# Kernel optimization log

Hardware: AMD Instinct MI355X
Metric: run time of the kernel (lower is better)

## Reference

```python
import jax, jax.numpy as jnp
import numpy as np

B, N, L, C, H = 2, 3000, 6, 128, 1
IN_DIM = 6
SIGMA_D = 1.0
EPS = 1e-5
DH = C // H


def _conv1(x, W, b):
    # pointwise Conv1d: x [B,Cin,N], W [Cout,Cin], b [Cout]
    return jnp.einsum('oc,bcn->bon', W, x) + b[None, :, None]


def _bn(x, g, beta):
    # BatchNorm1d (training-mode batch stats) over (B, N) per channel
    m = x.mean(axis=(0, 2), keepdims=True)
    v = x.var(axis=(0, 2), keepdims=True)
    return g[None, :, None] * (x - m) * jax.lax.rsqrt(v + EPS) + beta[None, :, None]


def setup_inputs() -> dict:
    key = jax.random.key(0)
    ks = iter(jax.random.split(key, 80))

    def w(shape, fan_in):
        return jax.random.normal(next(ks), shape, jnp.float32) * (1.0 / np.sqrt(fan_in))

    src = jax.random.normal(next(ks), (B, N, 3), jnp.float32)
    tgt = src + 0.1 * jax.random.normal(next(ks), (B, N, 3), jnp.float32)
    corr_pos = jnp.concatenate([src, tgt], axis=-1)  # [B,N,6]

    d = {
        'corr_pos': corr_pos, 'src_keypts': src, 'tgt_keypts': tgt,
        'init_W': w((C, IN_DIM), IN_DIM), 'init_b': jnp.zeros((C,), jnp.float32),
        'pcn_W': w((L, C, C), C), 'pcn_b': jnp.zeros((L, C), jnp.float32),
        'pcn_g': jnp.ones((L, C), jnp.float32), 'pcn_beta': jnp.zeros((L, C), jnp.float32),
        'qW': w((L, C, C), C), 'qb': jnp.zeros((L, C), jnp.float32),
        'kW': w((L, C, C), C), 'kb': jnp.zeros((L, C), jnp.float32),
        'vW': w((L, C, C), C), 'vb': jnp.zeros((L, C), jnp.float32),
        'm1W': w((L, C // 2, C), C), 'm1b': jnp.zeros((L, C // 2), jnp.float32),
        'm1g': jnp.ones((L, C // 2), jnp.float32), 'm1beta': jnp.zeros((L, C // 2), jnp.float32),
        'm2W': w((L, C // 2, C // 2), C // 2), 'm2b': jnp.zeros((L, C // 2), jnp.float32),
        'm2g': jnp.ones((L, C // 2), jnp.float32), 'm2beta': jnp.zeros((L, C // 2), jnp.float32),
        'm3W': w((L, C, C // 2), C // 2), 'm3b': jnp.zeros((L, C), jnp.float32),
        'c1W': w((32, C), C), 'c1b': jnp.zeros((32,), jnp.float32),
        'c2W': w((32, 32), 32), 'c2b': jnp.zeros((32,), jnp.float32),
        'c3W': w((1, 32), 32), 'c3b': jnp.zeros((1,), jnp.float32),
    }
    return d


def reference(corr_pos, src_keypts, tgt_keypts, init_W, init_b,
              pcn_W, pcn_b, pcn_g, pcn_beta,
              qW, qb, kW, kb, vW, vb,
              m1W, m1b, m1g, m1beta, m2W, m2b, m2g, m2beta, m3W, m3b,
              c1W, c1b, c2W, c2b, c3W, c3b):
    # spatial compatibility: clamp(1 - (d_src - d_tgt)^2 / sigma_d^2, min=0)  [B,N,N]
    src_dist = jnp.linalg.norm(src_keypts[:, :, None, :] - src_keypts[:, None, :, :], axis=-1)
    tgt_dist = jnp.linalg.norm(tgt_keypts[:, :, None, :] - tgt_keypts[:, None, :, :], axis=-1)
    sc = jnp.maximum(1.0 - (src_dist - tgt_dist) ** 2 / SIGMA_D ** 2, 0.0)

    # init embedding: [B,C,N]
    x = _conv1(jnp.swapaxes(corr_pos, 1, 2), init_W, init_b)
    scale = 1.0 / jnp.sqrt(jnp.float32(DH))

    for i in range(L):
        # PointCN layer
        x = jax.nn.relu(_bn(_conv1(x, pcn_W[i], pcn_b[i]), pcn_g[i], pcn_beta[i]))
        # NonLocal block
        Q = _conv1(x, qW[i], qb[i]).reshape(B, H, DH, N)
        K = _conv1(x, kW[i], kb[i]).reshape(B, H, DH, N)
        V = _conv1(x, vW[i], vb[i]).reshape(B, H, DH, N)
        scores = jnp.einsum('bhco,bhci->bhoi', Q, K) * scale  # [B,H,N,N]
        weight = jax.nn.softmax(sc[:, None, :, :] * scores, axis=-1)
        msg = jnp.einsum('bhoi,bhci->bhco', weight, V).reshape(B, C, N)
        msg = jax.nn.relu(_bn(_conv1(msg, m1W[i], m1b[i]), m1g[i], m1beta[i]))
        msg = jax.nn.relu(_bn(_conv1(msg, m2W[i], m2b[i]), m2g[i], m2beta[i]))
        msg = _conv1(msg, m3W[i], m3b[i])
        x = x + msg

    corr_feat = x
    norm = jnp.maximum(jnp.linalg.norm(corr_feat, axis=1, keepdims=True), 1e-12)
    normed_corr_feat = corr_feat / norm
    h = jax.nn.relu(_conv1(corr_feat, c1W, c1b))
    h = jax.nn.relu(_conv1(h, c2W, c2b))
    confidence = _conv1(h, c3W, c3b)[:, 0, :]  # [B,N]
    return confidence, normed_corr_feat
```

## Files before the change

### kernel.cpp

```cpp
#include <hip/hip_runtime.h>
#include <hip/hip_bf16.h>


#define BB 2
#define NN 3000
#define CC 128
#define LAYERS 6
#define BN_EPS 1e-5f
#define ATT_SCALE 0.08838834764831845f
#define INV_CNT (1.f / (float)(BB * NN))

typedef _Float16 f16;
typedef _Float16 f16x8 __attribute__((ext_vector_type(8)));
typedef float f32x4 __attribute__((ext_vector_type(4)));

__global__ void init_conv(const float* __restrict__ corr, const float* __restrict__ W,
                          const float* __restrict__ bias, float* __restrict__ x) {
  int idx = blockIdx.x * 256 + threadIdx.x;
  if (idx >= BB * CC * NN) return;
  int n = idx % NN;
  int c = (idx / NN) % CC;
  int b = idx / (NN * CC);
  const float* cp = corr + (b * NN + n) * 6;
  float acc = bias[c];
#pragma unroll
  for (int d = 0; d < 6; ++d) acc += W[c * 6 + d] * cp[d];
  x[idx] = acc;
}

template <int CIN, int COUT, int MODE, int INPT, int CSPLIT, int BNIN, int STATS>
__launch_bounds__(256)
__global__ void conv_k(const float* __restrict__ in, float* __restrict__ out,
                       const float* __restrict__ W, const float* __restrict__ bias,
                       const float* __restrict__ res,
                       const float* __restrict__ isums, const float* __restrict__ ig,
                       const float* __restrict__ ibeta,
                       const float* __restrict__ rsums, const float* __restrict__ rg,
                       const float* __restrict__ rbeta, float* __restrict__ osums) {
  constexpr int COB = COUT / CSPLIT;
  constexpr int CH = (CIN > 64) ? 64 : CIN;
  constexpr int KPT = COB / 32;
  __shared__ alignas(16) float Xs[CIN][INPT ? 36 : 32];
  __shared__ float Ws[COB][CH + 1];
  __shared__ float bnsc[BNIN ? CIN : 1], bnsh[BNIN ? CIN : 1];
  const int tid = threadIdx.x;
  const int p0 = blockIdx.x * 32;
  const int co0 = blockIdx.y * COB;

  if (BNIN) {
    for (int c = tid; c < CIN; c += 256) {
      float s = isums[c], s2 = isums[CIN + c];
      float mean = s * INV_CNT;
      float var = s2 * INV_CNT - mean * mean;
      float sc = ig[c] * rsqrtf(var + BN_EPS);
      bnsc[c] = sc;
      bnsh[c] = ibeta[c] - mean * sc;
    }
    __syncthreads();
  }

  if (INPT == 0) {
    for (int idx = tid; idx < CIN * 32; idx += 256) {
      int ci = idx >> 5, j = idx & 31;
      int p = p0 + j;
      float v = 0.f;
      if (p < BB * NN) {
        int b = p / NN, n = p % NN;
        v = in[(b * CIN + ci) * NN + n];
        if (BNIN) {
          v = v * bnsc[ci] + bnsh[ci];
          v = v > 0.f ? v : 0.f;
        }
      }
      Xs[ci][j] = v;
    }
  } else {
    for (int idx = tid; idx < CIN * 32; idx += 256) {
      int j = idx / CIN, ci = idx % CIN;
      int p = p0 + j;
      float v = 0.f;
      if (p < BB * NN) {
        v = in[p * CIN + ci];
        if (BNIN) {
          v = v * bnsc[ci] + bnsh[ci];
          v = v > 0.f ? v : 0.f;
        }
      }
      Xs[ci][j] = v;
    }
  }

  const int nb = (tid % 8) * 4;
  const int cb = (tid / 8) * KPT;

  float acc[KPT][4];
#pragma unroll
  for (int k = 0; k < KPT; ++k)
#pragma unroll
    for (int j = 0; j < 4; ++j) acc[k][j] = 0.f;

  for (int c0 = 0; c0 < CIN; c0 += CH) {
    __syncthreads();
    for (int idx = tid; idx < COB * CH; idx += 256) {
      int co = idx / CH, cc = idx % CH;
      Ws[co][cc] = W[(co0 + co) * CIN + c0 + cc];
    }
    __syncthreads();
#pragma unroll 4
    for (int cc = 0; cc < CH; ++cc) {
      float4 xv = *reinterpret_cast<const float4*>(&Xs[c0 + cc][nb]);
#pragma unroll
      for (int k = 0; k < KPT; ++k) {
        float w = Ws[cb + k][cc];
        acc[k][0] += w * xv.x;
        acc[k][1] += w * xv.y;
        acc[k][2] += w * xv.z;
        acc[k][3] += w * xv.w;
      }
    }
  }

#pragma unroll
  for (int k = 0; k < KPT; ++k) {
    int co = co0 + cb + k;
    float bv = bias[co];
    float rsc = 0.f, rsh = 0.f;
    if (MODE == 3) {
      float s = rsums[co], s2 = rsums[COUT + co];
      float mean = s * INV_CNT;
      float var = s2 * INV_CNT - mean * mean;
      rsc = rg[co] * rsqrtf(var + BN_EPS);
      rsh = rbeta[co] - mean * rsc;
    }
    float sp = 0.f, sp2 = 0.f;
#pragma unroll
    for (int j = 0; j < 4; ++j) {
      int p = p0 + nb + j;
      if (p < BB * NN) {
        int b = p / NN, n = p % NN;
        int o = (b * COUT + co) * NN + n;
        float v = acc[k][j] + bv;
        if (MODE == 1) v = v > 0.f ? v : 0.f;
        if (MODE == 3) {
          float rr = res[o] * rsc + rsh;
          v += (rr > 0.f ? rr : 0.f);
        }
        out[o] = v;
        if (STATS) {
          sp += v;
          sp2 += v * v;
        }
      }
    }
    if (STATS) {
      sp += __shfl_xor(sp, 1);
      sp2 += __shfl_xor(sp2, 1);
      sp += __shfl_xor(sp, 2);
      sp2 += __shfl_xor(sp2, 2);
      sp += __shfl_xor(sp, 4);
      sp2 += __shfl_xor(sp2, 4);
      if ((tid & 7) == 0) {
        atomicAdd(&osums[co], sp);
        atomicAdd(&osums[COUT + co], sp2);
      }
    }
  }
}

__launch_bounds__(256)
__global__ void conv_qkv(const float* __restrict__ Yp, const float* __restrict__ psums,
                         const float* __restrict__ pg, const float* __restrict__ pbeta,
                         const float* __restrict__ qW, const float* __restrict__ kW,
                         const float* __restrict__ vW, const float* __restrict__ qb,
                         const float* __restrict__ kb, const float* __restrict__ vb,
                         f16* __restrict__ Qh, f16* __restrict__ Ql,
                         f16* __restrict__ Kh, f16* __restrict__ Kl,
                         f16* __restrict__ Vh, f16* __restrict__ Vl) {
  __shared__ alignas(16) float Xs[128][32];
  __shared__ float Ws[64][65];
  __shared__ float bnsc[128], bnsh[128];
  const int tid = threadIdx.x;
  const int p0 = blockIdx.x * 32;
  const int sel = blockIdx.y >> 1;
  const int co0 = (blockIdx.y & 1) * 64;
  const float* W = (sel == 0) ? qW : (sel == 1) ? kW : vW;
  const float* bias = (sel == 0) ? qb : (sel == 1) ? kb : vb;

  for (int c = tid; c < 128; c += 256) {
    float s = psums[c], s2 = psums[128 + c];
    float mean = s * INV_CNT;
    float var = s2 * INV_CNT - mean * mean;
    float sc = pg[c] * rsqrtf(var + BN_EPS);
    bnsc[c] = sc;
    bnsh[c] = pbeta[c] - mean * sc;
  }
  __syncthreads();

  for (int idx = tid; idx < 128 * 32; idx += 256) {
    int ci = idx >> 5, j = idx & 31;
    int p = p0 + j;
    float v = 0.f;
    if (p < BB * NN) {
      int b = p / NN, n = p % NN;
      v = Yp[(b * 128 + ci) * NN + n];
      v = v * bnsc[ci] + bnsh[ci];
      v = v > 0.f ? v : 0.f;
    }
    Xs[ci][j] = v;
  }

  const int nb = (tid % 8) * 4;
  const int cb = (tid / 8) * 2;
  float acc[2][4] = {{0.f, 0.f, 0.f, 0.f}, {0.f, 0.f, 0.f, 0.f}};

  for (int c0 = 0; c0 < 128; c0 += 64) {
    __syncthreads();
    for (int idx = tid; idx < 64 * 64; idx += 256) {
      int co = idx >> 6, cc = idx & 63;
      Ws[co][cc] = W[(co0 + co) * 128 + c0 + cc];
    }
    __syncthreads();
#pragma unroll 4
    for (int cc = 0; cc < 64; ++cc) {
      float4 xv = *reinterpret_cast<const float4*>(&Xs[c0 + cc][nb]);
#pragma unroll
      for (int k = 0; k < 2; ++k) {
        float w = Ws[cb + k][cc];
        acc[k][0] += w * xv.x;
        acc[k][1] += w * xv.y;
        acc[k][2] += w * xv.z;
        acc[k][3] += w * xv.w;
      }
    }
  }

#pragma unroll
  for (int k = 0; k < 2; ++k) {
    int co = co0 + cb + k;
    float bv = bias[co];
#pragma unroll
    for (int j = 0; j < 4; ++j) {
      int p = p0 + nb + j;
      if (p < BB * NN) {
        int b = p / NN, n = p % NN;
        float v = acc[k][j] + bv;
        f16 h = (f16)v;
        f16 lo = (f16)(v - (float)h);
        if (sel == 0) {
          size_t o = (size_t)(b * NN + n) * CC + co;
          Qh[o] = h; Ql[o] = lo;
        } else if (sel == 1) {
          size_t o = (size_t)(b * NN + n) * CC + co;
          Kh[o] = h; Kl[o] = lo;
        } else {
          size_t o = (size_t)(b * CC + co) * NN + n;
          Vh[o] = h; Vl[o] = lo;
        }
      }
    }
  }
}

__launch_bounds__(256)
__global__ void attn_mf6(const f16* __restrict__ Qhp, const f16* __restrict__ Qlp,
                         const f16* __restrict__ Khp, const f16* __restrict__ Klp,
                         const f16* __restrict__ Vhp, const f16* __restrict__ Vlp,
                         const float* __restrict__ srcp, const float* __restrict__ tgtp,
                         float* __restrict__ pacc, float* __restrict__ pm,
                         float* __restrict__ pl, int chunk) {
  const int b = blockIdx.z;
  const int q0 = blockIdx.x * 64;
  const int s = blockIdx.y;
  const int cs = s * chunk;
  const int ce = min(cs + chunk, NN);
  const int tid = threadIdx.x;
  const int w = tid >> 6, lane = tid & 63, quad = lane >> 4, l15 = lane & 15;

  __shared__ f16 Ksh[32][136], Ksl[32][136];
  __shared__ f16 Vsh[128][40], Vsl[128][40];
  __shared__ f16 Ps[4][16][40];
  __shared__ float kps[6][36];

  float qp[4][6];
  const int orow = q0 + w * 16;
#pragma unroll
  for (int r = 0; r < 4; ++r) {
    int o = orow + quad * 4 + r;
    if (o >= NN) o = NN - 1;
#pragma unroll
    for (int d = 0; d < 3; ++d) {
      qp[r][d] = srcp[(b * NN + o) * 3 + d];
      qp[r][3 + d] = tgtp[(b * NN + o) * 3 + d];
    }
  }
  f16x8 qh[4], ql[4];
  {
    int o = orow + l15;
    if (o >= NN) o = NN - 1;
    size_t base = (size_t)(b * NN + o) * CC + quad * 8;
#pragma unroll
    for (int cc = 0; cc < 4; ++cc) {
      qh[cc] = *reinterpret_cast<const f16x8*>(Qhp + base + cc * 32);
      ql[cc] = *reinterpret_cast<const f16x8*>(Qlp + base + cc * 32);
    }
  }

  float m[4], l[4];
#pragma unroll
  for (int r = 0; r < 4; ++r) {
    m[r] = -1e30f;
    l[r] = 0.f;
  }
  f32x4 acco[8];
#pragma unroll
  for (int t = 0; t < 8; ++t) acco[t] = (f32x4){0.f, 0.f, 0.f, 0.f};

  const int NT = (ce - cs + 31) >> 5;
  for (int it = 0; it < NT; ++it) {
    const int kk0 = cs + it * 32;
    __syncthreads();
    for (int t = tid; t < 1024; t += 256) {
      int plane = t >> 9, row = (t >> 4) & 31, cu = t & 15;
      int kr = kk0 + row;
      if (kr >= NN) kr = NN - 1;
      const f16* src = (plane ? Klp : Khp) + (size_t)(b * NN + kr) * CC + cu * 8;
      uint4 v = *reinterpret_cast<const uint4*>(src);
      f16* dst = plane ? &Ksl[row][cu * 8] : &Ksh[row][cu * 8];
      *reinterpret_cast<uint4*>(dst) = v;
    }
    for (int t = tid; t < 1024; t += 256) {
      int plane = t >> 9, c = (t >> 2) & 127, iu = t & 3;
      int kb = kk0 + iu * 8;
      if (kb > NN - 8) kb = NN - 8;
      const f16* src = (plane ? Vlp : Vhp) + (size_t)(b * CC + c) * NN + kb;
      uint4 v = *reinterpret_cast<const uint4*>(src);
      f16* dst = plane ? &Vsl[c][iu * 8] : &Vsh[c][iu * 8];
      *reinterpret_cast<uint4*>(dst) = v;
    }
    for (int t = tid; t < 192; t += 256) {
      int d = t >> 5, i = t & 31;
      int ig = kk0 + i;
      if (ig >= NN) ig = NN - 1;
      kps[d][i] = (d < 3) ? srcp[(b * NN + ig) * 3 + d] : tgtp[(b * NN + ig) * 3 + d - 3];
    }
    __syncthreads();

    f32x4 accs[2];
#pragma unroll
    for (int k4 = 0; k4 < 2; ++k4) accs[k4] = (f32x4){0.f, 0.f, 0.f, 0.f};
#pragma unroll
    for (int cc = 0; cc < 4; ++cc) {
#pragma unroll
      for (int k4 = 0; k4 < 2; ++k4) {
        f16x8 bh = *reinterpret_cast<const f16x8*>(&Ksh[k4 * 16 + l15][cc * 32 + quad * 8]);
        f16x8 bl = *reinterpret_cast<const f16x8*>(&Ksl[k4 * 16 + l15][cc * 32 + quad * 8]);
        accs[k4] = __builtin_amdgcn_mfma_f32_16x16x32_f16(qh[cc], bl, accs[k4], 0, 0, 0);
        accs[k4] = __builtin_amdgcn_mfma_f32_16x16x32_f16(ql[cc], bh, accs[k4], 0, 0, 0);
        accs[k4] = __builtin_amdgcn_mfma_f32_16x16x32_f16(qh[cc], bh, accs[k4], 0, 0, 0);
      }
    }

    float sv[2][4];
#pragma unroll
    for (int k4 = 0; k4 < 2; ++k4) {
      int iloc = k4 * 16 + l15;
      int ig = kk0 + iloc;
      float kx = kps[0][iloc], ky = kps[1][iloc], kz = kps[2][iloc];
      float tx = kps[3][iloc], ty = kps[4][iloc], tz = kps[5][iloc];
#pragma unroll
      for (int r = 0; r < 4; ++r) {
        float dx = qp[r][0] - kx, dy = qp[r][1] - ky, dz = qp[r][2] - kz;
        float ds2 = dx * dx + dy * dy + dz * dz;
        float ex = qp[r][3] - tx, ey = qp[r][4] - ty, ez = qp[r][5] - tz;
        float dt2 = ex * ex + ey * ey + ez * ez;
        float d2 = ds2 + dt2 - 2.f * sqrtf(ds2 * dt2);
        float gg = 1.f - d2;
        gg = gg > 0.f ? gg : 0.f;
        float val = accs[k4][r] * (ATT_SCALE * gg);
        sv[k4][r] = (ig < ce) ? val : -1e30f;
      }
    }

    float tmax[4];
#pragma unroll
    for (int r = 0; r < 4; ++r) tmax[r] = fmaxf(sv[0][r], sv[1][r]);
#pragma unroll
    for (int d = 1; d <= 8; d <<= 1)
#pragma unroll
      for (int r = 0; r < 4; ++r) tmax[r] = fmaxf(tmax[r], __shfl_xor(tmax[r], d));

    float alpha[4], ps[4];
    f16 pf[2][4];
#pragma unroll
    for (int r = 0; r < 4; ++r) {
      float mn = fmaxf(m[r], tmax[r]);
      alpha[r] = __expf(m[r] - mn);
      m[r] = mn;
      pf[0][r] = (f16)__expf(sv[0][r] - mn);
      pf[1][r] = (f16)__expf(sv[1][r] - mn);
      ps[r] = (float)pf[0][r] + (float)pf[1][r];
    }
#pragma unroll
    for (int d = 1; d <= 8; d <<= 1)
#pragma unroll
      for (int r = 0; r < 4; ++r) ps[r] += __shfl_xor(ps[r], d);
#pragma unroll
    for (int r = 0; r < 4; ++r) {
      l[r] = l[r] * alpha[r] + ps[r];
#pragma unroll
      for (int t = 0; t < 8; ++t) acco[t][r] *= alpha[r];
    }
#pragma unroll
    for (int r = 0; r < 4; ++r) {
      Ps[w][quad * 4 + r][l15] = pf[0][r];
      Ps[w][quad * 4 + r][16 + l15] = pf[1][r];
    }
    __syncthreads();

    {
      f16x8 af = *reinterpret_cast<const f16x8*>(&Ps[w][l15][quad * 8]);
#pragma unroll
      for (int t = 0; t < 8; ++t) {
        f16x8 vh = *reinterpret_cast<const f16x8*>(&Vsh[t * 16 + l15][quad * 8]);
        f16x8 vl = *reinterpret_cast<const f16x8*>(&Vsl[t * 16 + l15][quad * 8]);
        acco[t] = __builtin_amdgcn_mfma_f32_16x16x32_f16(af, vl, acco[t], 0, 0, 0);
        acco[t] = __builtin_amdgcn_mfma_f32_16x16x32_f16(af, vh, acco[t], 0, 0, 0);
      }
    }
  }

  const int pidx = s * BB + b;
  if (l15 == 0) {
#pragma unroll
    for (int r = 0; r < 4; ++r) {
      int o = orow + quad * 4 + r;
      if (o < NN) {
        pm[pidx * NN + o] = m[r];
        pl[pidx * NN + o] = l[r];
      }
    }
  }
#pragma unroll
  for (int r = 0; r < 4; ++r) {
    int o = orow + quad * 4 + r;
    if (o < NN) {
      size_t base2 = ((size_t)pidx * NN + o) * CC;
#pragma unroll
      for (int t = 0; t < 8; ++t) pacc[base2 + t * 16 + l15] = acco[t][r];
    }
  }
}

__launch_bounds__(256)
__global__ void conv_m1(const float* __restrict__ pacc, const float* __restrict__ pm,
                        const float* __restrict__ pl, float* __restrict__ out,
                        const float* __restrict__ W, const float* __restrict__ bias,
                        float* __restrict__ osums, int ksplit) {
  __shared__ alignas(16) float Xs[128][36];
  __shared__ float Ws[64][65];
  __shared__ float Es[32][9];
  __shared__ float Li[32];
  const int tid = threadIdx.x;
  const int p0 = blockIdx.x * 32;

  if (tid < 32) {
    int p = p0 + tid;
    float Lv = 1.f;
    if (p < BB * NN) {
      int b = p / NN, o = p % NN;
      float M = -1e30f;
      for (int s = 0; s < ksplit; ++s) M = fmaxf(M, pm[(s * BB + b) * NN + o]);
      Lv = 0.f;
      for (int s = 0; s < ksplit; ++s) {
        int pi = s * BB + b;
        float e = __expf(pm[pi * NN + o] - M);
        Es[tid][s] = e;
        Lv += pl[pi * NN + o] * e;
      }
    } else {
      for (int s = 0; s < ksplit; ++s) Es[tid][s] = 0.f;
    }
    Li[tid] = 1.f / Lv;
  }
  __syncthreads();

  for (int idx = tid; idx < 1024; idx += 256) {
    int j = idx >> 5, c4 = (idx & 31) * 4;
    int p = p0 + j;
    float4 a = {0.f, 0.f, 0.f, 0.f};
    if (p < BB * NN) {
      int b = p / NN, o = p % NN;
      for (int s = 0; s < ksplit; ++s) {
        float e = Es[j][s];
        const float4 pv = *reinterpret_cast<const float4*>(
            &pacc[((size_t)(s * BB + b) * NN + o) * CC + c4]);
        a.x += pv.x * e;
        a.y += pv.y * e;
        a.z += pv.z * e;
        a.w += pv.w * e;
      }
      float inv = Li[j];
      a.x *= inv; a.y *= inv; a.z *= inv; a.w *= inv;
    }
    Xs[c4][j] = a.x;
    Xs[c4 + 1][j] = a.y;
    Xs[c4 + 2][j] = a.z;
    Xs[c4 + 3][j] = a.w;
  }

  const int nb = (tid % 8) * 4;
  const int cb = (tid / 8) * 2;
  float acc[2][4] = {{0.f, 0.f, 0.f, 0.f}, {0.f, 0.f, 0.f, 0.f}};

  for (int c0 = 0; c0 < 128; c0 += 64) {
    __syncthreads();
    for (int idx = tid; idx < 64 * 64; idx += 256) {
      int co = idx >> 6, cc = idx & 63;
      Ws[co][cc] = W[co * 128 + c0 + cc];
    }
    __syncthreads();
#pragma unroll 4
    for (int cc = 0; cc < 64; ++cc) {
      float4 xv = *reinterpret_cast<const float4*>(&Xs[c0 + cc][nb]);
#pragma unroll
      for (int k = 0; k < 2; ++k) {
        float w = Ws[cb + k][cc];
        acc[k][0] += w * xv.x;
        acc[k][1] += w * xv.y;
        acc[k][2] += w * xv.z;
        acc[k][3] += w * xv.w;
      }
    }
  }

#pragma unroll
  for (int k = 0; k < 2; ++k) {
    int co = cb + k;
    float bv = bias[co];
    float sp = 0.f, sp2 = 0.f;
#pragma unroll
    for (int j = 0; j < 4; ++j) {
      int p = p0 + nb + j;
      if (p < BB * NN) {
        int b = p / NN, n = p % NN;
        float v = acc[k][j] + bv;
        out[(b * 64 + co) * NN + n] = v;
        sp += v;
        sp2 += v * v;
      }
    }
    sp += __shfl_xor(sp, 1);
    sp2 += __shfl_xor(sp2, 1);
    sp += __shfl_xor(sp, 2);
    sp2 += __shfl_xor(sp2, 2);
    sp += __shfl_xor(sp, 4);
    sp2 += __shfl_xor(sp2, 4);
    if ((tid & 7) == 0) {
      atomicAdd(&osums[co], sp);
      atomicAdd(&osums[64 + co], sp2);
    }
  }
}

__launch_bounds__(256)
__global__ void head_all(const float* __restrict__ Xg,
                         const float* __restrict__ c1W, const float* __restrict__ c1b,
                         const float* __restrict__ c2W, const float* __restrict__ c2b,
                         const float* __restrict__ c3W, const float* __restrict__ c3b,
                         float* __restrict__ out) {
  __shared__ float Xs[128][33];
  __shared__ float W1[32][129];
  __shared__ float W2[32][33];
  __shared__ float Hs[32][33], H2s[32][33];
  __shared__ float Inv[32];
  const int tid = threadIdx.x;
  const int p0 = blockIdx.x * 32;
  const int j = tid >> 3, sub = tid & 7;

  for (int idx = tid; idx < 128 * 32; idx += 256) {
    int ci = idx >> 5, jj = idx & 31;
    int p = p0 + jj;
    float v = 0.f;
    if (p < BB * NN) {
      int b = p / NN, n = p % NN;
      v = Xg[(b * 128 + ci) * NN + n];
    }
    Xs[ci][jj] = v;
  }
  for (int idx = tid; idx < 32 * 128; idx += 256) {
    W1[idx >> 7][idx & 127] = c1W[idx];
  }
  for (int idx = tid; idx < 32 * 32; idx += 256) {
    W2[idx >> 5][idx & 31] = c2W[idx];
  }
  __syncthreads();

  {
    float h1v[4];
#pragma unroll
    for (int k = 0; k < 4; ++k) h1v[k] = c1b[sub * 4 + k];
    for (int ci = 0; ci < 128; ++ci) {
      float xv = Xs[ci][j];
#pragma unroll
      for (int k = 0; k < 4; ++k) h1v[k] += W1[sub * 4 + k][ci] * xv;
    }
#pragma unroll
    for (int k = 0; k < 4; ++k) Hs[j][sub * 4 + k] = h1v[k] > 0.f ? h1v[k] : 0.f;
  }
  __syncthreads();
  {
    float h2v[4];
#pragma unroll
    for (int k = 0; k < 4; ++k) h2v[k] = c2b[sub * 4 + k];
#pragma unroll
    for (int cc = 0; cc < 32; ++cc) {
      float hv = Hs[j][cc];
#pragma unroll
      for (int k = 0; k < 4; ++k) h2v[k] += W2[sub * 4 + k][cc] * hv;
    }
#pragma unroll
    for (int k = 0; k < 4; ++k) H2s[j][sub * 4 + k] = h2v[k] > 0.f ? h2v[k] : 0.f;
  }
  __syncthreads();

  float ssp = 0.f;
#pragma unroll
  for (int k = 0; k < 16; ++k) {
    float v = Xs[sub + 8 * k][j];
    ssp += v * v;
  }
  ssp += __shfl_xor(ssp, 1);
  ssp += __shfl_xor(ssp, 2);
  ssp += __shfl_xor(ssp, 4);

  if (sub == 0) {
    int p = p0 + j;
    if (p < BB * NN) {
      float conf = c3b[0];
#pragma unroll
      for (int c = 0; c < 32; ++c) conf += c3W[c] * H2s[j][c];
      out[p] = conf;
    }
    float nrm = sqrtf(ssp);
    nrm = nrm > 1e-12f ? nrm : 1e-12f;
    Inv[j] = 1.f / nrm;
  }
  __syncthreads();

  for (int idx = tid; idx < 128 * 32; idx += 256) {
    int c = idx >> 5, jj = idx & 31;
    int p = p0 + jj;
    if (p < BB * NN) {
      int b = p / NN, n = p % NN;
      out[BB * NN + (b * 128 + c) * NN + n] = Xs[c][jj] * Inv[jj];
    }
  }
}

extern "C" void kernel_launch(void* const* d_in, const int* in_sizes, int n_in,
                              void* d_out, int out_size, void* d_ws, size_t ws_size,
                              hipStream_t stream) {
  const float* corr = (const float*)d_in[0];
  const float* srcp = (const float*)d_in[1];
  const float* tgtp = (const float*)d_in[2];
  const float* initW = (const float*)d_in[3];
  const float* initb = (const float*)d_in[4];
  const float* pcnW = (const float*)d_in[5];
  const float* pcnb = (const float*)d_in[6];
  const float* pcng = (const float*)d_in[7];
  const float* pcnbeta = (const float*)d_in[8];
  const float* qW = (const float*)d_in[9];
  const float* qb = (const float*)d_in[10];
  const float* kW = (const float*)d_in[11];
  const float* kb = (const float*)d_in[12];
  const float* vW = (const float*)d_in[13];
  const float* vb = (const float*)d_in[14];
  const float* m1W = (const float*)d_in[15];
  const float* m1b = (const float*)d_in[16];
  const float* m1g = (const float*)d_in[17];
  const float* m1beta = (const float*)d_in[18];
  const float* m2W = (const float*)d_in[19];
  const float* m2b = (const float*)d_in[20];
  const float* m2g = (const float*)d_in[21];
  const float* m2beta = (const float*)d_in[22];
  const float* m3W = (const float*)d_in[23];
  const float* m3b = (const float*)d_in[24];
  const float* c1W = (const float*)d_in[25];
  const float* c1b = (const float*)d_in[26];
  const float* c2W = (const float*)d_in[27];
  const float* c2b = (const float*)d_in[28];
  const float* c3W = (const float*)d_in[29];
  const float* c3b = (const float*)d_in[30];

  const int FEAT = BB * CC * NN;
  const int PLANE = FEAT / 2;
  float* ws = (float*)d_ws;
  float* X = ws;
  float* Y = X + FEAT;
  float* QhF = Y + FEAT;
  float* QlF = QhF + PLANE;
  float* KhF = QlF + PLANE;
  float* KlF = KhF + PLANE;
  float* VhF = KlF + PLANE;
  float* VlF = VhF + PLANE;
  float* SB = VlF + PLANE;
  float* pacc = SB + 3072;
  f16* Qh = (f16*)QhF;
  f16* Ql = (f16*)QlF;
  f16* Kh = (f16*)KhF;
  f16* Kl = (f16*)KlF;
  f16* Vh = (f16*)VhF;
  f16* Vl = (f16*)VlF;
  float* T1 = QhF;
  float* T2 = KhF;

  const size_t base_f = (size_t)(2 * FEAT + 6 * PLANE + 3072);
  const size_t per_f = (size_t)BB * NN * CC + 2 * (size_t)BB * NN;
  int ksplit = 8;
  while (ksplit > 1 && (base_f + (size_t)ksplit * per_f) * 4 > ws_size) ksplit >>= 1;
  const int chunk = (((NN + ksplit - 1) / ksplit) + 7) & ~7;
  float* pm = pacc + (size_t)ksplit * BB * NN * CC;
  float* pl = pm + (size_t)ksplit * BB * NN;

  dim3 blk(256);
  const int PT = (BB * NN + 31) / 32;
  const int G_FEAT = (FEAT + 255) / 256;

  hipMemsetAsync(SB, 0, 3072 * sizeof(float), stream);
  init_conv<<<G_FEAT, blk, 0, stream>>>(corr, initW, initb, X);

  for (int i = 0; i < LAYERS; ++i) {
    float* pcnS = SB + i * 512;
    float* m1S = pcnS + 256;
    float* m2S = m1S + 128;
    conv_k<128, 128, 0, 0, 2, 0, 1><<<dim3(PT, 2), blk, 0, stream>>>(
        X, Y, pcnW + i * 16384, pcnb + i * 128, nullptr,
        nullptr, nullptr, nullptr, nullptr, nullptr, nullptr, pcnS);
    conv_qkv<<<dim3(PT, 6), blk, 0, stream>>>(
        Y, pcnS, pcng + i * 128, pcnbeta + i * 128, qW + i * 16384, kW + i * 16384,
        vW + i * 16384, qb + i * 128, kb + i * 128, vb + i * 128,
        Qh, Ql, Kh, Kl, Vh, Vl);
    attn_mf6<<<dim3((NN + 63) / 64, ksplit, BB), blk, 0, stream>>>(
        Qh, Ql, Kh, Kl, Vh, Vl, srcp, tgtp, pacc, pm, pl, chunk);
    conv_m1<<<PT, blk, 0, stream>>>(pacc, pm, pl, T1, m1W + i * 8192, m1b + i * 64,
                                    m1S, ksplit);
    conv_k<64, 64, 0, 0, 2, 1, 1><<<dim3(PT, 2), blk, 0, stream>>>(
        T1, T2, m2W + i * 4096, m2b + i * 64, nullptr,
        m1S, m1g + i * 64, m1beta + i * 64, nullptr, nullptr, nullptr, m2S);
    conv_k<64, 128, 3, 0, 2, 1, 0><<<dim3(PT, 2), blk, 0, stream>>>(
        T2, X, m3W + i * 8192, m3b + i * 128, Y,
        m2S, m2g + i * 64, m2beta + i * 64, pcnS, pcng + i * 128, pcnbeta + i * 128,
        nullptr);
  }

  head_all<<<PT, blk, 0, stream>>>(X, c1W, c1b, c2W, c2b, c3W, c3b, (float*)d_out);
}
```

Before: 1.508 ms.

## Shrink conv point tiles, widen attention blocks to 512 threads, raise ksplit

The conv kernels now take 16 points per block instead of 32, which doubles the grid for the small pointwise convs to fill more CUs. The m2 conv drops its output-channel split, and conv_m1 is retiled so each thread owns one output channel. The attention kernel grows to 512 threads covering 128 queries per block, so each K/V tile staged in shared memory is reused across twice as many queries. The key split rises to 16 to keep the grid large, at the cost of more partial-sum traffic in the merge step.

```diff
diff --git a/kernel.cpp b/kernel.cpp
--- a/kernel.cpp
+++ b/kernel.cpp
@@ -28,7 +28,7 @@
   x[idx] = acc;
 }
 
-template <int CIN, int COUT, int MODE, int INPT, int CSPLIT, int BNIN, int STATS>
+template <int CIN, int COUT, int NP, int MODE, int CSPLIT, int BNIN, int STATS>
 __launch_bounds__(256)
 __global__ void conv_k(const float* __restrict__ in, float* __restrict__ out,
                        const float* __restrict__ W, const float* __restrict__ bias,
@@ -39,12 +39,14 @@
                        const float* __restrict__ rbeta, float* __restrict__ osums) {
   constexpr int COB = COUT / CSPLIT;
   constexpr int CH = (CIN > 64) ? 64 : CIN;
-  constexpr int KPT = COB / 32;
-  __shared__ alignas(16) float Xs[CIN][INPT ? 36 : 32];
+  constexpr int PG = NP / 4;
+  constexpr int KPT = COB * PG / 256;
+  constexpr int XROW = (NP == 16) ? 20 : 32;
+  __shared__ alignas(16) float Xs[CIN][XROW];
   __shared__ float Ws[COB][CH + 1];
   __shared__ float bnsc[BNIN ? CIN : 1], bnsh[BNIN ? CIN : 1];
   const int tid = threadIdx.x;
-  const int p0 = blockIdx.x * 32;
+  const int p0 = blockIdx.x * NP;
   const int co0 = blockIdx.y * COB;
 
   if (BNIN) {
@@ -59,39 +61,23 @@
     __syncthreads();
   }
 
-  if (INPT == 0) {
-    for (int idx = tid; idx < CIN * 32; idx += 256) {
-      int ci = idx >> 5, j = idx & 31;
-      int p = p0 + j;
-      float v = 0.f;
-      if (p < BB * NN) {
-        int b = p / NN, n = p % NN;
-        v = in[(b * CIN + ci) * NN + n];
-        if (BNIN) {
-          v = v * bnsc[ci] + bnsh[ci];
-          v = v > 0.f ? v : 0.f;
-        }
-      }
-      Xs[ci][j] = v;
-    }
-  } else {
-    for (int idx = tid; idx < CIN * 32; idx += 256) {
-      int j = idx / CIN, ci = idx % CIN;
-      int p = p0 + j;
-      float v = 0.f;
-      if (p < BB * NN) {
-        v = in[p * CIN + ci];
-        if (BNIN) {
-          v = v * bnsc[ci] + bnsh[ci];
-          v = v > 0.f ? v : 0.f;
-        }
-      }
-      Xs[ci][j] = v;
-    }
-  }
-
-  const int nb = (tid % 8) * 4;
-  const int cb = (tid / 8) * KPT;
+  for (int idx = tid; idx < CIN * NP; idx += 256) {
+    int ci = idx / NP, j = idx % NP;
+    int p = p0 + j;
+    float v = 0.f;
+    if (p < BB * NN) {
+      int b = p / NN, n = p % NN;
+      v = in[(b * CIN + ci) * NN + n];
+      if (BNIN) {
+        v = v * bnsc[ci] + bnsh[ci];
+        v = v > 0.f ? v : 0.f;
+      }
+    }
+    Xs[ci][j] = v;
+  }
+
+  const int nb = (tid % PG) * 4;
+  const int cb = (tid / PG) * KPT;
 
   float acc[KPT][4];
 #pragma unroll
@@ -140,7 +126,6 @@
         int b = p / NN, n = p % NN;
         int o = (b * COUT + co) * NN + n;
         float v = acc[k][j] + bv;
-        if (MODE == 1) v = v > 0.f ? v : 0.f;
         if (MODE == 3) {
           float rr = res[o] * rsc + rsh;
           v += (rr > 0.f ? rr : 0.f);
@@ -153,13 +138,12 @@
       }
     }
     if (STATS) {
-      sp += __shfl_xor(sp, 1);
-      sp2 += __shfl_xor(sp2, 1);
-      sp += __shfl_xor(sp, 2);
-      sp2 += __shfl_xor(sp2, 2);
-      sp += __shfl_xor(sp, 4);
-      sp2 += __shfl_xor(sp2, 4);
-      if ((tid & 7) == 0) {
+#pragma unroll
+      for (int d = 1; d < PG; d <<= 1) {
+        sp += __shfl_xor(sp, d);
+        sp2 += __shfl_xor(sp2, d);
+      }
+      if ((tid & (PG - 1)) == 0) {
         atomicAdd(&osums[co], sp);
         atomicAdd(&osums[COUT + co], sp2);
       }
@@ -261,15 +245,15 @@
   }
 }
 
-__launch_bounds__(256)
-__global__ void attn_mf6(const f16* __restrict__ Qhp, const f16* __restrict__ Qlp,
+__launch_bounds__(512)
+__global__ void attn_mf7(const f16* __restrict__ Qhp, const f16* __restrict__ Qlp,
                          const f16* __restrict__ Khp, const f16* __restrict__ Klp,
                          const f16* __restrict__ Vhp, const f16* __restrict__ Vlp,
                          const float* __restrict__ srcp, const float* __restrict__ tgtp,
                          float* __restrict__ pacc, float* __restrict__ pm,
                          float* __restrict__ pl, int chunk) {
   const int b = blockIdx.z;
-  const int q0 = blockIdx.x * 64;
+  const int q0 = blockIdx.x * 128;
   const int s = blockIdx.y;
   const int cs = s * chunk;
   const int ce = min(cs + chunk, NN);
@@ -278,7 +262,7 @@
 
   __shared__ f16 Ksh[32][136], Ksl[32][136];
   __shared__ f16 Vsh[128][40], Vsl[128][40];
-  __shared__ f16 Ps[4][16][40];
+  __shared__ f16 Ps[8][16][40];
   __shared__ float kps[6][36];
 
   float qp[4][6];
@@ -319,7 +303,7 @@
   for (int it = 0; it < NT; ++it) {
     const int kk0 = cs + it * 32;
     __syncthreads();
-    for (int t = tid; t < 1024; t += 256) {
+    for (int t = tid; t < 1024; t += 512) {
       int plane = t >> 9, row = (t >> 4) & 31, cu = t & 15;
       int kr = kk0 + row;
       if (kr >= NN) kr = NN - 1;
@@ -328,7 +312,7 @@
       f16* dst = plane ? &Ksl[row][cu * 8] : &Ksh[row][cu * 8];
       *reinterpret_cast<uint4*>(dst) = v;
     }
-    for (int t = tid; t < 1024; t += 256) {
+    for (int t = tid; t < 1024; t += 512) {
       int plane = t >> 9, c = (t >> 2) & 127, iu = t & 3;
       int kb = kk0 + iu * 8;
       if (kb > NN - 8) kb = NN - 8;
@@ -337,8 +321,8 @@
       f16* dst = plane ? &Vsl[c][iu * 8] : &Vsh[c][iu * 8];
       *reinterpret_cast<uint4*>(dst) = v;
     }
-    for (int t = tid; t < 192; t += 256) {
-      int d = t >> 5, i = t & 31;
+    if (tid < 192) {
+      int d = tid >> 5, i = tid & 31;
       int ig = kk0 + i;
       if (ig >= NN) ig = NN - 1;
       kps[d][i] = (d < 3) ? srcp[(b * NN + ig) * 3 + d] : tgtp[(b * NN + ig) * 3 + d - 3];
@@ -456,14 +440,14 @@
                         const float* __restrict__ pl, float* __restrict__ out,
                         const float* __restrict__ W, const float* __restrict__ bias,
                         float* __restrict__ osums, int ksplit) {
-  __shared__ alignas(16) float Xs[128][36];
+  __shared__ alignas(16) float Xs[128][20];
   __shared__ float Ws[64][65];
-  __shared__ float Es[32][9];
-  __shared__ float Li[32];
+  __shared__ float Es[16][17];
+  __shared__ float Li[16];
   const int tid = threadIdx.x;
-  const int p0 = blockIdx.x * 32;
-
-  if (tid < 32) {
+  const int p0 = blockIdx.x * 16;
+
+  if (tid < 16) {
     int p = p0 + tid;
     float Lv = 1.f;
     if (p < BB * NN) {
@@ -484,7 +468,7 @@
   }
   __syncthreads();
 
-  for (int idx = tid; idx < 1024; idx += 256) {
+  for (int idx = tid; idx < 512; idx += 256) {
     int j = idx >> 5, c4 = (idx & 31) * 4;
     int p = p0 + j;
     float4 a = {0.f, 0.f, 0.f, 0.f};
@@ -508,34 +492,29 @@
     Xs[c4 + 3][j] = a.w;
   }
 
-  const int nb = (tid % 8) * 4;
-  const int cb = (tid / 8) * 2;
-  float acc[2][4] = {{0.f, 0.f, 0.f, 0.f}, {0.f, 0.f, 0.f, 0.f}};
+  const int nb = (tid & 3) * 4;
+  const int co = tid >> 2;
+  float acc[4] = {0.f, 0.f, 0.f, 0.f};
 
   for (int c0 = 0; c0 < 128; c0 += 64) {
     __syncthreads();
     for (int idx = tid; idx < 64 * 64; idx += 256) {
-      int co = idx >> 6, cc = idx & 63;
-      Ws[co][cc] = W[co * 128 + c0 + cc];
+      int cr = idx >> 6, cc = idx & 63;
+      Ws[cr][cc] = W[cr * 128 + c0 + cc];
     }
     __syncthreads();
 #pragma unroll 4
     for (int cc = 0; cc < 64; ++cc) {
       float4 xv = *reinterpret_cast<const float4*>(&Xs[c0 + cc][nb]);
-#pragma unroll
-      for (int k = 0; k < 2; ++k) {
-        float w = Ws[cb + k][cc];
-        acc[k][0] += w * xv.x;
-        acc[k][1] += w * xv.y;
-        acc[k][2] += w * xv.z;
-        acc[k][3] += w * xv.w;
-      }
-    }
-  }
-
-#pragma unroll
-  for (int k = 0; k < 2; ++k) {
-    int co = cb + k;
+      float w = Ws[co][cc];
+      acc[0] += w * xv.x;
+      acc[1] += w * xv.y;
+      acc[2] += w * xv.z;
+      acc[3] += w * xv.w;
+    }
+  }
+
+  {
     float bv = bias[co];
     float sp = 0.f, sp2 = 0.f;
 #pragma unroll
@@ -543,7 +522,7 @@
       int p = p0 + nb + j;
       if (p < BB * NN) {
         int b = p / NN, n = p % NN;
-        float v = acc[k][j] + bv;
+        float v = acc[j] + bv;
         out[(b * 64 + co) * NN + n] = v;
         sp += v;
         sp2 += v * v;
@@ -553,9 +532,7 @@
     sp2 += __shfl_xor(sp2, 1);
     sp += __shfl_xor(sp, 2);
     sp2 += __shfl_xor(sp2, 2);
-    sp += __shfl_xor(sp, 4);
-    sp2 += __shfl_xor(sp2, 4);
-    if ((tid & 7) == 0) {
+    if ((tid & 3) == 0) {
       atomicAdd(&osums[co], sp);
       atomicAdd(&osums[64 + co], sp2);
     }
@@ -716,14 +693,15 @@
 
   const size_t base_f = (size_t)(2 * FEAT + 6 * PLANE + 3072);
   const size_t per_f = (size_t)BB * NN * CC + 2 * (size_t)BB * NN;
-  int ksplit = 8;
+  int ksplit = 16;
   while (ksplit > 1 && (base_f + (size_t)ksplit * per_f) * 4 > ws_size) ksplit >>= 1;
   const int chunk = (((NN + ksplit - 1) / ksplit) + 7) & ~7;
   float* pm = pacc + (size_t)ksplit * BB * NN * CC;
   float* pl = pm + (size_t)ksplit * BB * NN;
 
   dim3 blk(256);
-  const int PT = (BB * NN + 31) / 32;
+  const int PT32 = (BB * NN + 31) / 32;
+  const int PT16 = (BB * NN + 15) / 16;
   const int G_FEAT = (FEAT + 255) / 256;
 
   hipMemsetAsync(SB, 0, 3072 * sizeof(float), stream);
@@ -733,25 +711,25 @@
     float* pcnS = SB + i * 512;
     float* m1S = pcnS + 256;
     float* m2S = m1S + 128;
-    conv_k<128, 128, 0, 0, 2, 0, 1><<<dim3(PT, 2), blk, 0, stream>>>(
+    conv_k<128, 128, 16, 0, 2, 0, 1><<<dim3(PT16, 2), blk, 0, stream>>>(
         X, Y, pcnW + i * 16384, pcnb + i * 128, nullptr,
         nullptr, nullptr, nullptr, nullptr, nullptr, nullptr, pcnS);
-    conv_qkv<<<dim3(PT, 6), blk, 0, stream>>>(
+    conv_qkv<<<dim3(PT32, 6), blk, 0, stream>>>(
         Y, pcnS, pcng + i * 128, pcnbeta + i * 128, qW + i * 16384, kW + i * 16384,
         vW + i * 16384, qb + i * 128, kb + i * 128, vb + i * 128,
         Qh, Ql, Kh, Kl, Vh, Vl);
-    attn_mf6<<<dim3((NN + 63) / 64, ksplit, BB), blk, 0, stream>>>(
+    attn_mf7<<<dim3((NN + 127) / 128, ksplit, BB), dim3(512), 0, stream>>>(
         Qh, Ql, Kh, Kl, Vh, Vl, srcp, tgtp, pacc, pm, pl, chunk);
-    conv_m1<<<PT, blk, 0, stream>>>(pacc, pm, pl, T1, m1W + i * 8192, m1b + i * 64,
-                                    m1S, ksplit);
-    conv_k<64, 64, 0, 0, 2, 1, 1><<<dim3(PT, 2), blk, 0, stream>>>(
+    conv_m1<<<PT16, blk, 0, stream>>>(pacc, pm, pl, T1, m1W + i * 8192, m1b + i * 64,
+                                      m1S, ksplit);
+    conv_k<64, 64, 16, 0, 1, 1, 1><<<dim3(PT16, 1), blk, 0, stream>>>(
         T1, T2, m2W + i * 4096, m2b + i * 64, nullptr,
         m1S, m1g + i * 64, m1beta + i * 64, nullptr, nullptr, nullptr, m2S);
-    conv_k<64, 128, 3, 0, 2, 1, 0><<<dim3(PT, 2), blk, 0, stream>>>(
+    conv_k<64, 128, 16, 3, 2, 1, 0><<<dim3(PT16, 2), blk, 0, stream>>>(
         T2, X, m3W + i * 8192, m3b + i * 128, Y,
         m2S, m2g + i * 64, m2beta + i * 64, pcnS, pcng + i * 128, pcnbeta + i * 128,
         nullptr);
   }
 
-  head_all<<<PT, blk, 0, stream>>>(X, c1W, c1b, c2W, c2b, c3W, c3b, (float*)d_out);
+  head_all<<<PT32, blk, 0, stream>>>(X, c1W, c1b, c2W, c2b, c3W, c3b, (float*)d_out);
 }
```

Measured after the change: 1.356 ms. 10.1% less time.
